# Kernel tuning notes

Measured on AMD Instinct MI355X. Metric: run time of the kernel, lower is better.

The kernel has to match this reference:

```python
import jax, jax.numpy as jnp
import numpy as np

D = 1024
H = 16
HD = D // H
SCALE = np.sqrt(HD).astype(np.float32)


def setup_inputs() -> dict:
    key = jax.random.key(0)
    ks = jax.random.split(key, 12)
    s = lambda fan_in: 1.0 / np.sqrt(fan_in)
    return {
        "x": jax.random.normal(ks[0], (4, 2048, D), dtype=jnp.float32),
        "qkv_w": jax.random.uniform(ks[1], (D, 3 * D), jnp.float32, -s(D), s(D)),
        "qkv_b": jax.random.uniform(ks[2], (3 * D,), jnp.float32, -s(D), s(D)),
        "out_w": jax.random.uniform(ks[3], (D, D), jnp.float32, -s(D), s(D)),
        "out_b": jax.random.uniform(ks[4], (D,), jnp.float32, -s(D), s(D)),
        "ln1_g": jnp.ones((D,), jnp.float32),
        "ln1_b": jnp.zeros((D,), jnp.float32),
        "ln2_g": jnp.ones((D,), jnp.float32),
        "ln2_b": jnp.zeros((D,), jnp.float32),
        "ffn_w1": jax.random.uniform(ks[5], (D, 4 * D), jnp.float32, -s(D), s(D)),
        "ffn_b1": jax.random.uniform(ks[6], (4 * D,), jnp.float32, -s(D), s(D)),
        "ffn_w2": jax.random.uniform(ks[7], (4 * D, D), jnp.float32, -s(4 * D), s(4 * D)),
        "ffn_b2": jax.random.uniform(ks[8], (D,), jnp.float32, -s(4 * D), s(4 * D)),
    }


def _layer_norm(x, g, b, eps=1e-5):
    mu = jnp.mean(x, axis=-1, keepdims=True)
    var = jnp.mean(jnp.square(x - mu), axis=-1, keepdims=True)
    return (x - mu) * jax.lax.rsqrt(var + eps) * g + b


def reference(x, qkv_w, qkv_b, out_w, out_b, ln1_g, ln1_b, ln2_g, ln2_b,
              ffn_w1, ffn_b1, ffn_w2, ffn_b2):
    B, L, C = x.shape
    h = _layer_norm(x, ln1_g, ln1_b)
    qkv = (h @ qkv_w + qkv_b).reshape(B, L, 3, H, HD)
    q = jnp.transpose(qkv[:, :, 0], (0, 2, 1, 3))  # [B,H,L,HD]
    k = jnp.transpose(qkv[:, :, 1], (0, 2, 1, 3))
    v = jnp.transpose(qkv[:, :, 2], (0, 2, 1, 3))
    attn = jnp.einsum("bhqd,bhkd->bhqk", q, k) / SCALE
    attn = jax.nn.softmax(attn, axis=-1)
    o = jnp.einsum("bhqk,bhkd->bhqd", attn, v)
    o = jnp.transpose(o, (0, 2, 1, 3)).reshape(B, L, C)
    o = o @ out_w + out_b
    out = _layer_norm(o, ln2_g, ln2_b)
    ffn = jax.nn.gelu(out @ ffn_w1 + ffn_b1, approximate=False) @ ffn_w2 + ffn_b2
    return out + ffn
```

## Files before the change

kernel.cpp:

```cpp
#include <hip/hip_runtime.h>
#include <hip/hip_bf16.h>
#include <math.h>

typedef __bf16 bf16_t;
typedef __bf16 bf16x8 __attribute__((ext_vector_type(8)));
typedef __bf16 bf16x4 __attribute__((ext_vector_type(4)));
typedef float  f32x4  __attribute__((ext_vector_type(4)));
typedef float  f32x16 __attribute__((ext_vector_type(16)));
typedef unsigned int u32x2 __attribute__((ext_vector_type(2)));
typedef unsigned int u32x4 __attribute__((ext_vector_type(4)));

#define MFMA_BF16(a, b, c) __builtin_amdgcn_mfma_f32_16x16x32_bf16(a, b, c, 0, 0, 0)
#define MFMA32_BF16(a, b, c) __builtin_amdgcn_mfma_f32_32x32x16_bf16(a, b, c, 0, 0, 0)

#if __has_builtin(__builtin_amdgcn_exp2f)
__device__ __forceinline__ float fast_exp2(float x) { return __builtin_amdgcn_exp2f(x); }
#else
__device__ __forceinline__ float fast_exp2(float x) { return exp2f(x); }
#endif

__device__ __forceinline__ float fast_gelu(float v) {
  const float u = v * (1.f + 0.044715f * v * v);
  const float tt = fast_exp2(2.3022078f * u);
  return v - v / (tt + 1.f);
}

__device__ __forceinline__ void gload_lds16(const bf16_t* g, bf16_t* l) {
  __builtin_amdgcn_global_load_lds(
      (const __attribute__((address_space(1))) void*)g,
      (__attribute__((address_space(3))) void*)l, 16, 0, 0);
}

__global__ __launch_bounds__(256) void sa_transpose4(const float* __restrict__ s0, bf16_t* __restrict__ d0,
                                                     const float* __restrict__ s1, bf16_t* __restrict__ d1,
                                                     const float* __restrict__ s2, bf16_t* __restrict__ d2,
                                                     const float* __restrict__ s3, bf16_t* __restrict__ d3) {
  __shared__ bf16_t tile[64][65];
  const int bid = blockIdx.x;
  const float* in; bf16_t* out; int K, N, local;
  if (bid < 768)       { in = s0; out = d0; K = 1024; N = 3072; local = bid; }
  else if (bid < 1024) { in = s1; out = d1; K = 1024; N = 1024; local = bid - 768; }
  else if (bid < 2048) { in = s2; out = d2; K = 1024; N = 4096; local = bid - 1024; }
  else                 { in = s3; out = d3; K = 4096; N = 1024; local = bid - 2048; }
  const int nx = N >> 6;
  const int n0 = (local % nx) * 64, k0 = (local / nx) * 64;
  const int t = threadIdx.x;
#pragma unroll
  for (int i = 0; i < 16; ++i) {
    int idx = t + i * 256;
    int r = idx >> 6, c = idx & 63;
    tile[r][c] = (bf16_t)in[(size_t)(k0 + r) * N + n0 + c];
  }
  __syncthreads();
#pragma unroll
  for (int i = 0; i < 16; ++i) {
    int idx = t + i * 256;
    int r = idx >> 6, c = idx & 63;
    out[(size_t)(n0 + r) * K + k0 + c] = tile[c][r];
  }
}

__global__ __launch_bounds__(256) void sa_layernorm(const float* __restrict__ in,
                                                    const float* __restrict__ gamma,
                                                    const float* __restrict__ beta,
                                                    bf16_t* __restrict__ out_bf) {
  const int row = blockIdx.x, t = threadIdx.x;
  const float4 v = *(const float4*)(in + (size_t)row * 1024 + t * 4);
  float s  = v.x + v.y + v.z + v.w;
  float ss = v.x * v.x + v.y * v.y + v.z * v.z + v.w * v.w;
#pragma unroll
  for (int m = 1; m < 64; m <<= 1) {
    s  += __shfl_xor(s, m, 64);
    ss += __shfl_xor(ss, m, 64);
  }
  __shared__ float red[8];
  const int w = t >> 6, lane = t & 63;
  if (lane == 0) { red[w] = s; red[4 + w] = ss; }
  __syncthreads();
  s  = red[0] + red[1] + red[2] + red[3];
  ss = red[4] + red[5] + red[6] + red[7];
  const float mu   = s * (1.f / 1024.f);
  const float rstd = rsqrtf(ss * (1.f / 1024.f) - mu * mu + 1e-5f);
  const float4 gv = *(const float4*)(gamma + t * 4);
  const float4 bv = *(const float4*)(beta + t * 4);
  bf16x4 ob = { (bf16_t)((v.x - mu) * rstd * gv.x + bv.x),
                (bf16_t)((v.y - mu) * rstd * gv.y + bv.y),
                (bf16_t)((v.z - mu) * rstd * gv.z + bv.z),
                (bf16_t)((v.w - mu) * rstd * gv.w + bv.w) };
  *(bf16x4*)(out_bf + (size_t)row * 1024 + t * 4) = ob;
}

__global__ __launch_bounds__(256) void sa_layernorm_b(const bf16_t* __restrict__ in,
                                                      const float* __restrict__ gamma,
                                                      const float* __restrict__ beta,
                                                      bf16_t* __restrict__ out_bf) {
  const int row = blockIdx.x, t = threadIdx.x;
  const bf16x4 iv = *(const bf16x4*)(in + (size_t)row * 1024 + t * 4);
  const float v0 = (float)iv[0], v1 = (float)iv[1], v2 = (float)iv[2], v3 = (float)iv[3];
  float s  = v0 + v1 + v2 + v3;
  float ss = v0 * v0 + v1 * v1 + v2 * v2 + v3 * v3;
#pragma unroll
  for (int m = 1; m < 64; m <<= 1) {
    s  += __shfl_xor(s, m, 64);
    ss += __shfl_xor(ss, m, 64);
  }
  __shared__ float red[8];
  const int w = t >> 6, lane = t & 63;
  if (lane == 0) { red[w] = s; red[4 + w] = ss; }
  __syncthreads();
  s  = red[0] + red[1] + red[2] + red[3];
  ss = red[4] + red[5] + red[6] + red[7];
  const float mu   = s * (1.f / 1024.f);
  const float rstd = rsqrtf(ss * (1.f / 1024.f) - mu * mu + 1e-5f);
  const float4 gv = *(const float4*)(gamma + t * 4);
  const float4 bv = *(const float4*)(beta + t * 4);
  bf16x4 ob = { (bf16_t)((v0 - mu) * rstd * gv.x + bv.x),
                (bf16_t)((v1 - mu) * rstd * gv.y + bv.y),
                (bf16_t)((v2 - mu) * rstd * gv.z + bv.z),
                (bf16_t)((v3 - mu) * rstd * gv.w + bv.w) };
  *(bf16x4*)(out_bf + (size_t)row * 1024 + t * 4) = ob;
}

template <int EPI>
__global__ __launch_bounds__(256, 2) void sa_gemm4(const bf16_t* __restrict__ A,
                                                   const bf16_t* __restrict__ Bt,
                                                   const float* __restrict__ bias,
                                                   int K, int N,
                                                   float* __restrict__ fout,
                                                   bf16_t* __restrict__ bfout,
                                                   const bf16_t* __restrict__ res,
                                                   bf16_t* __restrict__ qb,
                                                   bf16_t* __restrict__ kb,
                                                   bf16_t* __restrict__ vb) {
  __shared__ __attribute__((aligned(16))) bf16_t As[2][128][64];
  __shared__ __attribute__((aligned(16))) bf16_t Bs[2][128][64];

  const int gx = gridDim.x;
  const int flat = blockIdx.y * gx + blockIdx.x;
  const int c = flat & 7;
  const int local = flat >> 3;
  const int sg = local >> 6;
  const int rem = local & 63;
  const int by = c * 8 + (rem >> 3);
  const int bx = sg * 8 + (rem & 7);

  const int m0 = by * 128, n0 = bx * 128;
  const int t = threadIdx.x;
  const int w = t >> 6, lane = t & 63;
  const int wr = w >> 1, wc = w & 1;
  const int fr = lane & 15, fq = lane >> 4;
  const int swz = fr & 7;
  const int srow = lane >> 3;
  const int scol = ((lane & 7) ^ srow) * 8;
  const int NT = K >> 6;

  const f32x4 fzero = { 0.f, 0.f, 0.f, 0.f };
  f32x4 acc[4][4];
#pragma unroll
  for (int mi = 0; mi < 4; ++mi)
#pragma unroll
    for (int ni = 0; ni < 4; ++ni) acc[mi][ni] = fzero;

  auto stage = [&](int tt, int sb) {
#pragma unroll
    for (int i = 0; i < 4; ++i) {
      const int ch = w * 4 + i;
      const int row = ch * 8 + srow;
      gload_lds16(A  + (size_t)(m0 + row) * K + tt * 64 + scol, &As[sb][ch * 8][0]);
      gload_lds16(Bt + (size_t)(n0 + row) * K + tt * 64 + scol, &Bs[sb][ch * 8][0]);
    }
  };

  auto compute = [&](auto curc) {
    constexpr int cur = decltype(curc)::value;
    bf16x8 af[4][2], bfr[4][2];
#pragma unroll
    for (int mi = 0; mi < 4; ++mi)
#pragma unroll
      for (int kk = 0; kk < 2; ++kk)
        af[mi][kk] = *(const bf16x8*)&As[cur][wr * 64 + mi * 16 + fr][((kk * 4 + fq) ^ swz) * 8];
#pragma unroll
    for (int ni = 0; ni < 4; ++ni)
#pragma unroll
      for (int kk = 0; kk < 2; ++kk)
        bfr[ni][kk] = *(const bf16x8*)&Bs[cur][wc * 64 + ni * 16 + fr][((kk * 4 + fq) ^ swz) * 8];
    __builtin_amdgcn_s_setprio(1);
#pragma unroll
    for (int kk = 0; kk < 2; ++kk)
#pragma unroll
      for (int mi = 0; mi < 4; ++mi)
#pragma unroll
        for (int ni = 0; ni < 4; ++ni)
          acc[mi][ni] = MFMA_BF16(af[mi][kk], bfr[ni][kk], acc[mi][ni]);
    __builtin_amdgcn_s_setprio(0);
  };

  stage(0, 0);
  __syncthreads();

  for (int tt = 0; tt < NT; tt += 2) {
    stage(tt + 1, 1);
    compute(std::integral_constant<int, 0>{});
    __syncthreads();
    if (tt + 2 < NT) stage(tt + 2, 0);
    compute(std::integral_constant<int, 1>{});
    __syncthreads();
  }

#pragma unroll
  for (int ni = 0; ni < 4; ++ni) {
    const int n = n0 + wc * 64 + ni * 16 + fr;
    const float bn = bias[n];
#pragma unroll
    for (int mi = 0; mi < 4; ++mi) {
      const int mbase = m0 + wr * 64 + mi * 16 + fq * 4;
      float vv[4];
#pragma unroll
      for (int r = 0; r < 4; ++r) vv[r] = acc[mi][ni][r] + bn;
      if constexpr (EPI == 0) {
        const int which = n >> 10;
        const int hh = (n >> 6) & 15;
        const int d = n & 63;
        const int b = mbase >> 11, l = mbase & 2047;
        if (which == 0) {
#pragma unroll
          for (int r = 0; r < 4; ++r)
            qb[((size_t)(b * 16 + hh) * 2048 + l + r) * 64 + d] =
                (bf16_t)(vv[r] * (0.125f * 1.44269504088896340736f));
        } else if (which == 1) {
#pragma unroll
          for (int r = 0; r < 4; ++r)
            kb[((size_t)(b * 16 + hh) * 2048 + l + r) * 64 + d] = (bf16_t)vv[r];
        } else {
          bf16x4 pv = { (bf16_t)vv[0], (bf16_t)vv[1], (bf16_t)vv[2], (bf16_t)vv[3] };
          *(bf16x4*)(vb + ((size_t)(b * 16 + hh) * 64 + d) * 2048 + l) = pv;
        }
      } else if constexpr (EPI == 1) {
#pragma unroll
        for (int r = 0; r < 4; ++r)
          bfout[(size_t)(mbase + r) * N + n] = (bf16_t)vv[r];
      } else if constexpr (EPI == 2) {
#pragma unroll
        for (int r = 0; r < 4; ++r)
          bfout[(size_t)(mbase + r) * N + n] = (bf16_t)fast_gelu(vv[r]);
      } else {
#pragma unroll
        for (int r = 0; r < 4; ++r)
          fout[(size_t)(mbase + r) * N + n] = vv[r] + (float)res[(size_t)(mbase + r) * N + n];
      }
    }
  }
}

__global__ __launch_bounds__(256) void sa_attn32(const bf16_t* __restrict__ qb,
                                                 const bf16_t* __restrict__ kb,
                                                 const bf16_t* __restrict__ vb,
                                                 bf16_t* __restrict__ out) {
  __shared__ __attribute__((aligned(16))) bf16_t Ks[64][64];
  __shared__ __attribute__((aligned(16))) bf16_t Vt[64][64];

  const int nwg = gridDim.x * gridDim.y;
  const int flat = blockIdx.y * gridDim.x + blockIdx.x;
  const int wg = (flat & 7) * (nwg >> 3) + (flat >> 3);
  const int qblk = wg & 15, bh = wg >> 4;

  const int t = threadIdx.x, wq = t >> 6, lane = t & 63;
  const int q31 = lane & 31, hi = lane >> 5;
  const int qx = q31 & 7;
  const size_t base = (size_t)bh * 2048 * 64;

  const int row0 = t >> 3, u0 = t & 7;
  const int sc = (u0 ^ (row0 & 7)) * 8;
  const int gc = u0 * 8;

  const bf16_t* qrow = qb + base + (size_t)(qblk * 128 + wq * 32 + q31) * 64 + hi * 8;
  bf16x8 qf[4];
#pragma unroll
  for (int c = 0; c < 4; ++c) qf[c] = *(const bf16x8*)(qrow + c * 16);

  bf16x8 kreg0, kreg1, vreg0, vreg1;
  kreg0 = *(const bf16x8*)(kb + base + (size_t)row0 * 64 + gc);
  kreg1 = *(const bf16x8*)(kb + base + (size_t)(row0 + 32) * 64 + gc);
  vreg0 = *(const bf16x8*)(vb + base + (size_t)row0 * 2048 + gc);
  vreg1 = *(const bf16x8*)(vb + base + (size_t)(row0 + 32) * 2048 + gc);

  f32x16 o0, o1;
#pragma unroll
  for (int i = 0; i < 16; ++i) { o0[i] = 0.f; o1[i] = 0.f; }
  float lsum = 0.f;

  for (int kv0 = 0; kv0 < 2048; kv0 += 64) {
    __syncthreads();
    *(bf16x8*)&Ks[row0][sc] = kreg0;
    *(bf16x8*)&Ks[row0 + 32][sc] = kreg1;
    *(bf16x8*)&Vt[row0][sc] = vreg0;
    *(bf16x8*)&Vt[row0 + 32][sc] = vreg1;
    if (kv0 + 64 < 2048) {
      const int kvn = kv0 + 64;
      kreg0 = *(const bf16x8*)(kb + base + (size_t)(kvn + row0) * 64 + gc);
      kreg1 = *(const bf16x8*)(kb + base + (size_t)(kvn + row0 + 32) * 64 + gc);
      vreg0 = *(const bf16x8*)(vb + base + (size_t)row0 * 2048 + kvn + gc);
      vreg1 = *(const bf16x8*)(vb + base + (size_t)(row0 + 32) * 2048 + kvn + gc);
    }
    __syncthreads();

    f32x16 s0, s1;
#pragma unroll
    for (int i = 0; i < 16; ++i) { s0[i] = 0.f; s1[i] = 0.f; }
    __builtin_amdgcn_s_setprio(1);
#pragma unroll
    for (int c = 0; c < 4; ++c) {
      bf16x8 ka0 = *(const bf16x8*)&Ks[q31]     [((2 * c + hi) ^ qx) * 8];
      bf16x8 ka1 = *(const bf16x8*)&Ks[q31 + 32][((2 * c + hi) ^ qx) * 8];
      s0 = MFMA32_BF16(ka0, qf[c], s0);
      s1 = MFMA32_BF16(ka1, qf[c], s1);
    }
    __builtin_amdgcn_s_setprio(0);

#pragma unroll
    for (int i = 0; i < 16; ++i) { s0[i] = fast_exp2(s0[i]); lsum += s0[i]; }
#pragma unroll
    for (int i = 0; i < 16; ++i) { s1[i] = fast_exp2(s1[i]); lsum += s1[i]; }

    u32x4 pw[4];
#define PACK_CHUNK(c, SB, off)                                                      \
    {                                                                               \
      unsigned int x0, x1, y0, y1;                                                  \
      asm("v_cvt_pk_bf16_f32 %0, %1, %2" : "=v"(x0) : "v"(SB[off+0]), "v"(SB[off+1])); \
      asm("v_cvt_pk_bf16_f32 %0, %1, %2" : "=v"(x1) : "v"(SB[off+2]), "v"(SB[off+3])); \
      asm("v_cvt_pk_bf16_f32 %0, %1, %2" : "=v"(y0) : "v"(SB[off+4]), "v"(SB[off+5])); \
      asm("v_cvt_pk_bf16_f32 %0, %1, %2" : "=v"(y1) : "v"(SB[off+6]), "v"(SB[off+7])); \
      u32x2 r0 = __builtin_amdgcn_permlane32_swap(x0, y0, false, false);            \
      u32x2 r1 = __builtin_amdgcn_permlane32_swap(x1, y1, false, false);            \
      pw[c][0] = r0[0]; pw[c][1] = r1[0]; pw[c][2] = r0[1]; pw[c][3] = r1[1];       \
    }
    PACK_CHUNK(0, s0, 0)
    PACK_CHUNK(1, s0, 8)
    PACK_CHUNK(2, s1, 0)
    PACK_CHUNK(3, s1, 8)
#undef PACK_CHUNK

    __builtin_amdgcn_s_setprio(1);
#pragma unroll
    for (int c = 0; c < 4; ++c) {
      bf16x8 pf = *(const bf16x8*)&pw[c];
      bf16x8 va0 = *(const bf16x8*)&Vt[q31]     [((2 * c + hi) ^ qx) * 8];
      bf16x8 va1 = *(const bf16x8*)&Vt[q31 + 32][((2 * c + hi) ^ qx) * 8];
      o0 = MFMA32_BF16(va0, pf, o0);
      o1 = MFMA32_BF16(va1, pf, o1);
    }
    __builtin_amdgcn_s_setprio(0);
  }

  lsum += __shfl_xor(lsum, 32, 64);
  const float linv = 1.f / lsum;
  const int b = bh >> 4, h = bh & 15;
  const int qg = qblk * 128 + wq * 32 + q31;
  bf16_t* orow = out + (size_t)(b * 2048 + qg) * 1024 + h * 64;
#pragma unroll
  for (int rg = 0; rg < 4; ++rg) {
    bf16x4 olo = { (bf16_t)(o0[4 * rg + 0] * linv), (bf16_t)(o0[4 * rg + 1] * linv),
                   (bf16_t)(o0[4 * rg + 2] * linv), (bf16_t)(o0[4 * rg + 3] * linv) };
    *(bf16x4*)(orow + 8 * rg + 4 * hi) = olo;
    bf16x4 ohi = { (bf16_t)(o1[4 * rg + 0] * linv), (bf16_t)(o1[4 * rg + 1] * linv),
                   (bf16_t)(o1[4 * rg + 2] * linv), (bf16_t)(o1[4 * rg + 3] * linv) };
    *(bf16x4*)(orow + 32 + 8 * rg + 4 * hi) = ohi;
  }
}

extern "C" void kernel_launch(void* const* d_in, const int* in_sizes, int n_in,
                              void* d_out, int out_size, void* d_ws, size_t ws_size,
                              hipStream_t stream) {
  const float* x      = (const float*)d_in[0];
  const float* qkv_w  = (const float*)d_in[1];
  const float* qkv_b  = (const float*)d_in[2];
  const float* out_w  = (const float*)d_in[3];
  const float* out_b  = (const float*)d_in[4];
  const float* ln1_g  = (const float*)d_in[5];
  const float* ln1_b  = (const float*)d_in[6];
  const float* ln2_g  = (const float*)d_in[7];
  const float* ln2_b  = (const float*)d_in[8];
  const float* ffn_w1 = (const float*)d_in[9];
  const float* ffn_b1 = (const float*)d_in[10];
  const float* ffn_w2 = (const float*)d_in[11];
  const float* ffn_b2 = (const float*)d_in[12];
  float* outp = (float*)d_out;

  char* p = (char*)d_ws;
  auto alloc = [&](size_t bytes) { char* r = p; p += bytes; return r; };
  bf16_t* qkvw_t = (bf16_t*)alloc((size_t)3072 * 1024 * 2);
  bf16_t* outw_t = (bf16_t*)alloc((size_t)1024 * 1024 * 2);
  bf16_t* w1_t   = (bf16_t*)alloc((size_t)4096 * 1024 * 2);
  bf16_t* w2_t   = (bf16_t*)alloc((size_t)1024 * 4096 * 2);
  bf16_t* h_bf   = (bf16_t*)alloc((size_t)8192 * 1024 * 2);
  bf16_t* q_buf  = (bf16_t*)alloc((size_t)8192 * 1024 * 2);
  bf16_t* k_buf  = (bf16_t*)alloc((size_t)8192 * 1024 * 2);
  bf16_t* v_buf  = (bf16_t*)alloc((size_t)8192 * 1024 * 2);
  bf16_t* a_bf   = (bf16_t*)alloc((size_t)8192 * 1024 * 2);
  bf16_t* o_bf   = (bf16_t*)alloc((size_t)8192 * 1024 * 2);
  bf16_t* out_bf = (bf16_t*)alloc((size_t)8192 * 1024 * 2);
  bf16_t* t_bf   = (bf16_t*)alloc((size_t)8192 * 4096 * 2);

  sa_transpose4<<<3072, 256, 0, stream>>>(qkv_w, qkvw_t, out_w, outw_t,
                                          ffn_w1, w1_t, ffn_w2, w2_t);

  sa_layernorm<<<8192, 256, 0, stream>>>(x, ln1_g, ln1_b, h_bf);

  sa_gemm4<0><<<dim3(3072 / 128, 8192 / 128), 256, 0, stream>>>(
      h_bf, qkvw_t, qkv_b, 1024, 3072, nullptr, nullptr, nullptr, q_buf, k_buf, v_buf);

  sa_attn32<<<dim3(16, 64), 256, 0, stream>>>(q_buf, k_buf, v_buf, a_bf);

  sa_gemm4<1><<<dim3(1024 / 128, 8192 / 128), 256, 0, stream>>>(
      a_bf, outw_t, out_b, 1024, 1024, nullptr, o_bf, nullptr, nullptr, nullptr, nullptr);

  sa_layernorm_b<<<8192, 256, 0, stream>>>(o_bf, ln2_g, ln2_b, out_bf);

  sa_gemm4<2><<<dim3(4096 / 128, 8192 / 128), 256, 0, stream>>>(
      out_bf, w1_t, ffn_b1, 1024, 4096, nullptr, t_bf, nullptr, nullptr, nullptr, nullptr);

  sa_gemm4<3><<<dim3(1024 / 128, 8192 / 128), 256, 0, stream>>>(
      t_bf, w2_t, ffn_b2, 4096, 1024, outp, nullptr, out_bf, nullptr, nullptr, nullptr);
}
```

Before: 369.2 us.

## Double-buffer K/V shared tiles in attention and vectorize row-sum accumulation

The attention kernel now keeps two K/V tiles in shared memory. Each iteration writes the next tile into the idle buffer while computing on the current one, so there is one barrier per tile instead of two. The serial scalar softmax-sum chain is replaced by two 16-wide vector accumulators that are reduced once after the loop, which shortens the dependency chain. In exchange, shared memory per block doubles, which may reduce occupancy, and register pressure rises from the extra accumulators.

New measurement: 366.3 us. Within noise of the previous version (-0.8%).

```diff
diff --git a/kernel.cpp b/kernel.cpp
--- a/kernel.cpp
+++ b/kernel.cpp
@@ -1,6 +1,7 @@
 #include <hip/hip_runtime.h>
 #include <hip/hip_bf16.h>
 #include <math.h>
+#include <type_traits>
 
 typedef __bf16 bf16_t;
 typedef __bf16 bf16x8 __attribute__((ext_vector_type(8)));
@@ -256,8 +257,8 @@
                                                  const bf16_t* __restrict__ kb,
                                                  const bf16_t* __restrict__ vb,
                                                  bf16_t* __restrict__ out) {
-  __shared__ __attribute__((aligned(16))) bf16_t Ks[64][64];
-  __shared__ __attribute__((aligned(16))) bf16_t Vt[64][64];
+  __shared__ __attribute__((aligned(16))) bf16_t Ks[2][64][64];
+  __shared__ __attribute__((aligned(16))) bf16_t Vt[2][64][64];
 
   const int nwg = gridDim.x * gridDim.y;
   const int flat = blockIdx.y * gridDim.x + blockIdx.x;
@@ -278,49 +279,44 @@
 #pragma unroll
   for (int c = 0; c < 4; ++c) qf[c] = *(const bf16x8*)(qrow + c * 16);
 
-  bf16x8 kreg0, kreg1, vreg0, vreg1;
-  kreg0 = *(const bf16x8*)(kb + base + (size_t)row0 * 64 + gc);
-  kreg1 = *(const bf16x8*)(kb + base + (size_t)(row0 + 32) * 64 + gc);
-  vreg0 = *(const bf16x8*)(vb + base + (size_t)row0 * 2048 + gc);
-  vreg1 = *(const bf16x8*)(vb + base + (size_t)(row0 + 32) * 2048 + gc);
-
-  f32x16 o0, o1;
-#pragma unroll
-  for (int i = 0; i < 16; ++i) { o0[i] = 0.f; o1[i] = 0.f; }
-  float lsum = 0.f;
-
-  for (int kv0 = 0; kv0 < 2048; kv0 += 64) {
-    __syncthreads();
-    *(bf16x8*)&Ks[row0][sc] = kreg0;
-    *(bf16x8*)&Ks[row0 + 32][sc] = kreg1;
-    *(bf16x8*)&Vt[row0][sc] = vreg0;
-    *(bf16x8*)&Vt[row0 + 32][sc] = vreg1;
-    if (kv0 + 64 < 2048) {
-      const int kvn = kv0 + 64;
-      kreg0 = *(const bf16x8*)(kb + base + (size_t)(kvn + row0) * 64 + gc);
-      kreg1 = *(const bf16x8*)(kb + base + (size_t)(kvn + row0 + 32) * 64 + gc);
-      vreg0 = *(const bf16x8*)(vb + base + (size_t)row0 * 2048 + kvn + gc);
-      vreg1 = *(const bf16x8*)(vb + base + (size_t)(row0 + 32) * 2048 + kvn + gc);
-    }
-    __syncthreads();
-
+  const bf16_t* kp0 = kb + base + (size_t)row0 * 64 + gc;
+  const bf16_t* kp1 = kb + base + (size_t)(row0 + 32) * 64 + gc;
+  const bf16_t* vp0 = vb + base + (size_t)row0 * 2048 + gc;
+  const bf16_t* vp1 = vb + base + (size_t)(row0 + 32) * 2048 + gc;
+
+  bf16x8 kr0, kr1, vr0, vr1;
+  auto LOAD = [&]() {
+    kr0 = *(const bf16x8*)kp0;  kp0 += 64 * 64;
+    kr1 = *(const bf16x8*)kp1;  kp1 += 64 * 64;
+    vr0 = *(const bf16x8*)vp0;  vp0 += 64;
+    vr1 = *(const bf16x8*)vp1;  vp1 += 64;
+  };
+
+  f32x16 o0, o1, la0, la1;
+#pragma unroll
+  for (int i = 0; i < 16; ++i) { o0[i] = 0.f; o1[i] = 0.f; la0[i] = 0.f; la1[i] = 0.f; }
+
+  auto COMPUTE = [&](auto bufc) {
+    constexpr int buf = decltype(bufc)::value;
     f32x16 s0, s1;
 #pragma unroll
     for (int i = 0; i < 16; ++i) { s0[i] = 0.f; s1[i] = 0.f; }
     __builtin_amdgcn_s_setprio(1);
 #pragma unroll
     for (int c = 0; c < 4; ++c) {
-      bf16x8 ka0 = *(const bf16x8*)&Ks[q31]     [((2 * c + hi) ^ qx) * 8];
-      bf16x8 ka1 = *(const bf16x8*)&Ks[q31 + 32][((2 * c + hi) ^ qx) * 8];
+      bf16x8 ka0 = *(const bf16x8*)&Ks[buf][q31]     [((2 * c + hi) ^ qx) * 8];
+      bf16x8 ka1 = *(const bf16x8*)&Ks[buf][q31 + 32][((2 * c + hi) ^ qx) * 8];
       s0 = MFMA32_BF16(ka0, qf[c], s0);
       s1 = MFMA32_BF16(ka1, qf[c], s1);
     }
     __builtin_amdgcn_s_setprio(0);
 
 #pragma unroll
-    for (int i = 0; i < 16; ++i) { s0[i] = fast_exp2(s0[i]); lsum += s0[i]; }
-#pragma unroll
-    for (int i = 0; i < 16; ++i) { s1[i] = fast_exp2(s1[i]); lsum += s1[i]; }
+    for (int i = 0; i < 16; ++i) s0[i] = fast_exp2(s0[i]);
+#pragma unroll
+    for (int i = 0; i < 16; ++i) s1[i] = fast_exp2(s1[i]);
+    la0 += s0;
+    la1 += s1;
 
     u32x4 pw[4];
 #define PACK_CHUNK(c, SB, off)                                                      \
@@ -344,14 +340,49 @@
 #pragma unroll
     for (int c = 0; c < 4; ++c) {
       bf16x8 pf = *(const bf16x8*)&pw[c];
-      bf16x8 va0 = *(const bf16x8*)&Vt[q31]     [((2 * c + hi) ^ qx) * 8];
-      bf16x8 va1 = *(const bf16x8*)&Vt[q31 + 32][((2 * c + hi) ^ qx) * 8];
+      bf16x8 va0 = *(const bf16x8*)&Vt[buf][q31]     [((2 * c + hi) ^ qx) * 8];
+      bf16x8 va1 = *(const bf16x8*)&Vt[buf][q31 + 32][((2 * c + hi) ^ qx) * 8];
       o0 = MFMA32_BF16(va0, pf, o0);
       o1 = MFMA32_BF16(va1, pf, o1);
     }
     __builtin_amdgcn_s_setprio(0);
-  }
-
+  };
+
+  auto STORE = [&](auto bufc) {
+    constexpr int buf = decltype(bufc)::value;
+    *(bf16x8*)&Ks[buf][row0][sc] = kr0;
+    *(bf16x8*)&Ks[buf][row0 + 32][sc] = kr1;
+    *(bf16x8*)&Vt[buf][row0][sc] = vr0;
+    *(bf16x8*)&Vt[buf][row0 + 32][sc] = vr1;
+  };
+
+  LOAD();
+  STORE(std::integral_constant<int, 0>{});
+  LOAD();
+  __syncthreads();
+
+  for (int it = 0; it < 32; it += 2) {
+    STORE(std::integral_constant<int, 1>{});
+    if (it + 2 < 32) LOAD();
+    COMPUTE(std::integral_constant<int, 0>{});
+    __syncthreads();
+    if (it + 2 < 32) {
+      STORE(std::integral_constant<int, 0>{});
+      if (it + 3 < 32) LOAD();
+    }
+    COMPUTE(std::integral_constant<int, 1>{});
+    __syncthreads();
+  }
+
+  f32x16 lt = la0 + la1;
+  float lsum = 0.f;
+  {
+    float p0 = (lt[0] + lt[1]) + (lt[2] + lt[3]);
+    float p1 = (lt[4] + lt[5]) + (lt[6] + lt[7]);
+    float p2 = (lt[8] + lt[9]) + (lt[10] + lt[11]);
+    float p3 = (lt[12] + lt[13]) + (lt[14] + lt[15]);
+    lsum = (p0 + p1) + (p2 + p3);
+  }
   lsum += __shfl_xor(lsum, 32, 64);
   const float linv = 1.f / lsum;
   const int b = bh >> 4, h = bh & 15;
```
